# Kernel tuning notes

Hardware: AMD Instinct MI355X
Metric: run time of the kernel (lower is better)

## Reference

```python
import jax, jax.numpy as jnp
import numpy as np

BS, SEQ_Q = 16, 2048
ATTN_DIM, K_DIM, HEAD, RANK = 1024, 1024, 16, 16
A_H = ATTN_DIM // HEAD        # 64
K_R = K_DIM // RANK           # 64
HR = HEAD * RANK              # 256
EXP = 2
EPS = 1e-5


def setup_inputs() -> dict:
    key = jax.random.key(0)
    ks = jax.random.split(key, 12)
    n = lambda k, shape, scale=1.0: jax.random.normal(k, shape, dtype=jnp.float32) * scale
    lin = ATTN_DIM ** -0.5
    xav = (2.0 / (K_R + RANK)) ** 0.5  # xavier_normal for factor
    return {
        "Q": n(ks[0], (BS, SEQ_Q, ATTN_DIM)),
        "K": n(ks[1], (BS, K_DIM, ATTN_DIM)),
        "V": n(ks[2], (BS, K_DIM, ATTN_DIM)),
        "WQ": n(ks[3], (ATTN_DIM, ATTN_DIM), lin), "bQ": jnp.zeros((ATTN_DIM,), jnp.float32),
        "WK": n(ks[4], (ATTN_DIM, ATTN_DIM), lin), "bK": jnp.zeros((ATTN_DIM,), jnp.float32),
        "WV": n(ks[5], (ATTN_DIM, ATTN_DIM), lin), "bV": jnp.zeros((ATTN_DIM,), jnp.float32),
        "factor": n(ks[6], (1, A_H, K_R, RANK), xav),
        "W1": n(ks[7], (EXP * ATTN_DIM, ATTN_DIM), lin), "b1": jnp.zeros((EXP * ATTN_DIM,), jnp.float32),
        "W2": n(ks[8], (ATTN_DIM, EXP * ATTN_DIM), (EXP * ATTN_DIM) ** -0.5), "b2": jnp.zeros((ATTN_DIM,), jnp.float32),
        "gamma": jnp.ones((ATTN_DIM,), jnp.float32),
        "beta": jnp.zeros((ATTN_DIM,), jnp.float32),
    }


def reference(Q, K, V, WQ, bQ, WK, bK, WV, bV, factor, W1, b1, W2, b2, gamma, beta):
    bs = Q.shape[0]
    fac = factor[0]  # [a_h, k_r, rank]
    # Q path: [bs, a_h, head*rank, seq_q/rank]
    q = (Q @ WQ.T + bQ).reshape(bs, A_H, HR, -1)
    # K/V path: low-rank projection via learned factor -> [bs, a_h, head*rank, rank]
    k = jnp.einsum('bahk,akr->bahr', (K @ WK.T + bK).reshape(bs, A_H, HR, K_R), fac)
    v = jnp.einsum('bahk,akr->bahr', (V @ WV.T + bV).reshape(bs, A_H, HR, K_R), fac)
    # scores: Q^T K / sqrt(head*rank) -> [bs, a_h, L, rank]
    scores = jnp.einsum('bahl,bahr->balr', q, k) / jnp.float32(HR) ** 0.5
    attn = jax.nn.softmax(scores, axis=-1)
    # attn @ V^T -> [bs, a_h, L, head*rank], then flatten back to [bs, seq_q, attn_dim]
    ctx = jnp.einsum('balr,bahr->balh', attn, v).reshape(bs, -1, ATTN_DIM)
    # FFN (dropout = identity in eval)
    h = jax.nn.relu(ctx @ W1.T + b1)
    y = h @ W2.T + b2
    # residual + LayerNorm
    x = y + Q
    mu = jnp.mean(x, axis=-1, keepdims=True)
    var = jnp.var(x, axis=-1, keepdims=True)
    return (x - mu) * jax.lax.rsqrt(var + EPS) * gamma + beta
```

## Files before the change

### kernel.cpp

```cpp
#include <hip/hip_runtime.h>
#include <cstdint>

typedef unsigned short u16;
typedef unsigned int   u32;
typedef u16    u16x4  __attribute__((ext_vector_type(4)));
typedef u16    u16x8  __attribute__((ext_vector_type(8)));
typedef __bf16 bf16x8 __attribute__((ext_vector_type(8)));
typedef float  f32x4  __attribute__((ext_vector_type(4)));

__device__ __forceinline__ u16 f2b(float x) {
  u32 u = __builtin_bit_cast(u32, x);
  u32 r = (u + 0x7fffu + ((u >> 16) & 1u)) >> 16;
  return (u16)r;
}
__device__ __forceinline__ float b2f(u16 u) {
  return __builtin_bit_cast(float, (u32)u << 16);
}

__device__ __forceinline__ void gl2lds16(const u16* g, u16* l) {
  __builtin_amdgcn_global_load_lds(
      (__attribute__((address_space(1))) void*)g,
      (__attribute__((address_space(3))) void*)l, 16, 0, 0);
}

__global__ __launch_bounds__(256) void cvt_f32_bf16(
    const float* __restrict__ in, u16* __restrict__ out, long n)
{
  long i = ((long)blockIdx.x * 256 + threadIdx.x) * 4;
  if (i >= n) return;
  f32x4 v = *(const f32x4*)&in[i];
  u16x4 o = { f2b(v[0]), f2b(v[1]), f2b(v[2]), f2b(v[3]) };
  *(u16x4*)&out[i] = o;
}

#define BM 128
#define BN 128
#define BKK 32

__global__ __launch_bounds__(256) void gemm_bt(
    const u16* __restrict__ A, const u16* __restrict__ B,
    const float* __restrict__ bias, u16* __restrict__ C,
    int M, int N, int K, int relu)
{
  __shared__ __attribute__((aligned(16))) u16 As[BM * BKK];
  __shared__ __attribute__((aligned(16))) u16 Bs[BN * BKK];

  const int tid  = threadIdx.x;
  const int lane = tid & 63;
  const int wave = tid >> 6;
  const int lr   = lane & 15;
  const int quad = lane >> 4;
  const int wm = (wave >> 1) * 64;
  const int wn = (wave & 1) * 64;

  const long m0 = (long)blockIdx.y * BM;
  const long n0 = (long)blockIdx.x * BN;

  const int c1  = tid + 256;
  const int ar0 = tid >> 2, ac0 = (tid & 3) * 8;
  const int ar1 = c1 >> 2,  ac1 = (c1 & 3) * 8;

  const u16* Ab = A + m0 * K;
  const u16* Bb = B + n0 * K;

  f32x4 acc[4][4] = {};

  for (int k0 = 0; k0 < K; k0 += BKK) {
    __syncthreads();
    gl2lds16(Ab + (long)ar0 * K + (k0 + ac0), &As[tid * 8]);
    gl2lds16(Ab + (long)ar1 * K + (k0 + ac1), &As[c1 * 8]);
    gl2lds16(Bb + (long)ar0 * K + (k0 + ac0), &Bs[tid * 8]);
    gl2lds16(Bb + (long)ar1 * K + (k0 + ac1), &Bs[c1 * 8]);
    __syncthreads();

    bf16x8 af[4], bff[4];
#pragma unroll
    for (int i = 0; i < 4; ++i)
      af[i] = *(const bf16x8*)&As[(wm + i * 16 + lr) * BKK + quad * 8];
#pragma unroll
    for (int i = 0; i < 4; ++i)
      bff[i] = *(const bf16x8*)&Bs[(wn + i * 16 + lr) * BKK + quad * 8];
#pragma unroll
    for (int i = 0; i < 4; ++i)
#pragma unroll
      for (int j = 0; j < 4; ++j)
        acc[i][j] = __builtin_amdgcn_mfma_f32_16x16x32_bf16(af[i], bff[j], acc[i][j], 0, 0, 0);
  }

#pragma unroll
  for (int j = 0; j < 4; ++j) {
    const int col = wn + j * 16 + lr;
    const float bv = bias[n0 + col];
#pragma unroll
    for (int i = 0; i < 4; ++i) {
#pragma unroll
      for (int r = 0; r < 4; ++r) {
        const int row = wm + i * 16 + quad * 4 + r;
        float v = acc[i][j][r] + bv;
        if (relu) v = fmaxf(v, 0.0f);
        C[(m0 + row) * (long)N + (n0 + col)] = f2b(v);
      }
    }
  }
}

__global__ __launch_bounds__(256) void attn_kernel(
    const u16* __restrict__ Qp, const u16* __restrict__ Kp,
    const u16* __restrict__ Vp, const float* __restrict__ factor,
    u16* __restrict__ Ctx)
{
  __shared__ __attribute__((aligned(16))) float fac_s[64 * 16];
  __shared__ __attribute__((aligned(16))) float k_s[256][20];
  __shared__ __attribute__((aligned(16))) float v_s[256][20];
  __shared__ __attribute__((aligned(16))) float s_s[128][20];

  const int t = threadIdx.x;
  const int b = blockIdx.x >> 6;
  const int a = blockIdx.x & 63;

  for (int i = t; i < 1024; i += 256) fac_s[i] = factor[a * 1024 + i];
  __syncthreads();

  {
    const long kb = (((long)(b * 1024 + a * 16)) << 10) + (long)t * 64;
    float kacc[16] = {}, vacc[16] = {};
    for (int kk8 = 0; kk8 < 64; kk8 += 8) {
      u16x8 kv8 = *(const u16x8*)&Kp[kb + kk8];
      u16x8 vv8 = *(const u16x8*)&Vp[kb + kk8];
#pragma unroll
      for (int j = 0; j < 8; ++j) {
        const float kv = b2f(kv8[j]), vv = b2f(vv8[j]);
        const float* fr = &fac_s[(kk8 + j) * 16];
#pragma unroll
        for (int r = 0; r < 16; ++r) { kacc[r] += kv * fr[r]; vacc[r] += vv * fr[r]; }
      }
    }
#pragma unroll
    for (int r = 0; r < 16; ++r) { k_s[t][r] = kacc[r] * 0.0625f; v_s[t][r] = vacc[r]; }
  }
  __syncthreads();

  {
    const int l = t & 127, half = t >> 7;
    const long qb = (((long)(b * 2048 + a * 32)) << 10) + l;
    f32x4 acc0 = {}, acc1 = {};
    for (int h = 0; h < 256; ++h) {
      const float qv = b2f(Qp[qb + (long)h * 128]);
      f32x4 k0 = *(const f32x4*)&k_s[h][half * 8];
      f32x4 k1 = *(const f32x4*)&k_s[h][half * 8 + 4];
      acc0 += k0 * qv;
      acc1 += k1 * qv;
    }
    *(f32x4*)&s_s[l][half * 8]     = acc0;
    *(f32x4*)&s_s[l][half * 8 + 4] = acc1;
  }
  __syncthreads();

  if (t < 128) {
    float vals[16];
    float m = -1e30f;
#pragma unroll
    for (int r = 0; r < 16; ++r) { vals[r] = s_s[t][r]; m = fmaxf(m, vals[r]); }
    float sum = 0.0f;
#pragma unroll
    for (int r = 0; r < 16; ++r) { vals[r] = __expf(vals[r] - m); sum += vals[r]; }
    const float inv = 1.0f / sum;
#pragma unroll
    for (int r = 0; r < 16; ++r) s_s[t][r] = vals[r] * inv;
  }
  __syncthreads();

  {
    f32x4 v0 = *(const f32x4*)&v_s[t][0];
    f32x4 v1 = *(const f32x4*)&v_s[t][4];
    f32x4 v2 = *(const f32x4*)&v_s[t][8];
    f32x4 v3 = *(const f32x4*)&v_s[t][12];
    const long cb = (((long)(b * 2048 + a * 32)) << 10) + t;
    for (int l = 0; l < 128; ++l) {
      f32x4 a0 = *(const f32x4*)&s_s[l][0];
      f32x4 a1 = *(const f32x4*)&s_s[l][4];
      f32x4 a2 = *(const f32x4*)&s_s[l][8];
      f32x4 a3 = *(const f32x4*)&s_s[l][12];
      f32x4 p = a0 * v0 + a1 * v1 + a2 * v2 + a3 * v3;
      Ctx[cb + (long)l * 256] = f2b(p[0] + p[1] + p[2] + p[3]);
    }
  }
}

__global__ __launch_bounds__(256) void ln_kernel(
    const u16* __restrict__ Y, const float* __restrict__ Qin,
    const float* __restrict__ gamma, const float* __restrict__ beta,
    float* __restrict__ out)
{
  const long row = blockIdx.x;
  const int t = threadIdx.x;
  const long base = (row << 10) + (long)t * 4;

  u16x4 y4 = *(const u16x4*)&Y[base];
  f32x4 q4 = *(const f32x4*)&Qin[base];
  f32x4 x;
#pragma unroll
  for (int c = 0; c < 4; ++c) x[c] = b2f(y4[c]) + q4[c];

  float s  = x[0] + x[1] + x[2] + x[3];
  float sq = x[0]*x[0] + x[1]*x[1] + x[2]*x[2] + x[3]*x[3];
#pragma unroll
  for (int o = 1; o < 64; o <<= 1) {
    s  += __shfl_xor(s, o);
    sq += __shfl_xor(sq, o);
  }
  __shared__ float red[8];
  if ((t & 63) == 0) { red[(t >> 6) * 2] = s; red[(t >> 6) * 2 + 1] = sq; }
  __syncthreads();
  s  = red[0] + red[2] + red[4] + red[6];
  sq = red[1] + red[3] + red[5] + red[7];

  const float mean = s * (1.0f / 1024.0f);
  const float var  = sq * (1.0f / 1024.0f) - mean * mean;
  const float rstd = rsqrtf(var + 1e-5f);

  f32x4 g4 = *(const f32x4*)&gamma[t * 4];
  f32x4 be4 = *(const f32x4*)&beta[t * 4];
  f32x4 o4;
#pragma unroll
  for (int c = 0; c < 4; ++c) o4[c] = (x[c] - mean) * rstd * g4[c] + be4[c];
  *(f32x4*)&out[base] = o4;
}

extern "C" void kernel_launch(void* const* d_in, const int* in_sizes, int n_in,
                              void* d_out, int out_size, void* d_ws, size_t ws_size,
                              hipStream_t stream)
{
  (void)in_sizes; (void)n_in; (void)out_size; (void)ws_size;
  const float* Q      = (const float*)d_in[0];
  const float* K      = (const float*)d_in[1];
  const float* V      = (const float*)d_in[2];
  const float* WQ     = (const float*)d_in[3];
  const float* bQ     = (const float*)d_in[4];
  const float* WK     = (const float*)d_in[5];
  const float* bK     = (const float*)d_in[6];
  const float* WV     = (const float*)d_in[7];
  const float* bV     = (const float*)d_in[8];
  const float* factor = (const float*)d_in[9];
  const float* W1     = (const float*)d_in[10];
  const float* b1     = (const float*)d_in[11];
  const float* W2     = (const float*)d_in[12];
  const float* b2     = (const float*)d_in[13];
  const float* gamma  = (const float*)d_in[14];
  const float* beta   = (const float*)d_in[15];
  float* out = (float*)d_out;

  const long NQ = 33554432L;
  const long NK = 16777216L;
  const long ND = 1048576L;
  const long NW = 2097152L;

  char* w = (char*)d_ws;
  u16* Qb  = (u16*)(w);
  u16* Kb  = (u16*)(w + 67108864L);
  u16* Vb  = (u16*)(w + 100663296L);
  u16* WQb = (u16*)(w + 134217728L);
  u16* WKb = (u16*)(w + 136314880L);
  u16* WVb = (u16*)(w + 138412032L);
  u16* W1b = (u16*)(w + 140509184L);
  u16* W2b = (u16*)(w + 144703488L);
  u16* Qp  = (u16*)(w + 148897792L);
  u16* Kp  = (u16*)(w + 216006656L);
  u16* Vp  = (u16*)(w + 249561088L);
  u16* Ctx = (u16*)(w + 283115520L);
  u16* Hb  = (u16*)(w);
  u16* Yb  = (u16*)(w + 216006656L);

  cvt_f32_bf16<<<(int)(NQ / 1024), 256, 0, stream>>>(Q,  Qb,  NQ);
  cvt_f32_bf16<<<(int)(NK / 1024), 256, 0, stream>>>(K,  Kb,  NK);
  cvt_f32_bf16<<<(int)(NK / 1024), 256, 0, stream>>>(V,  Vb,  NK);
  cvt_f32_bf16<<<(int)(ND / 1024), 256, 0, stream>>>(WQ, WQb, ND);
  cvt_f32_bf16<<<(int)(ND / 1024), 256, 0, stream>>>(WK, WKb, ND);
  cvt_f32_bf16<<<(int)(ND / 1024), 256, 0, stream>>>(WV, WVb, ND);
  cvt_f32_bf16<<<(int)(NW / 1024), 256, 0, stream>>>(W1, W1b, NW);
  cvt_f32_bf16<<<(int)(NW / 1024), 256, 0, stream>>>(W2, W2b, NW);

  gemm_bt<<<dim3(8, 256),  256, 0, stream>>>(Qb, WQb, bQ, Qp, 32768, 1024, 1024, 0);
  gemm_bt<<<dim3(8, 128),  256, 0, stream>>>(Kb, WKb, bK, Kp, 16384, 1024, 1024, 0);
  gemm_bt<<<dim3(8, 128),  256, 0, stream>>>(Vb, WVb, bV, Vp, 16384, 1024, 1024, 0);

  attn_kernel<<<1024, 256, 0, stream>>>(Qp, Kp, Vp, factor, Ctx);

  gemm_bt<<<dim3(16, 256), 256, 0, stream>>>(Ctx, W1b, b1, Hb, 32768, 2048, 1024, 1);
  gemm_bt<<<dim3(8, 256),  256, 0, stream>>>(Hb, W2b, b2, Yb, 32768, 1024, 2048, 0);

  ln_kernel<<<32768, 256, 0, stream>>>(Yb, Q, gamma, beta, out);
}
```

Before: 1.120 ms.

## Merge conversion launches, deepen GEMM K-tile, swizzle LDS, group block order

The eight fp32-to-bf16 conversion launches become one kernel that uses segment offsets to pick the source and destination. The GEMM K-tile doubles from 32 to 64, halving the number of barrier pairs per output tile. LDS rows get an XOR swizzle to avoid bank conflicts on the 128-byte row stride. Blocks are remapped so groups of eight M-tiles run together for better L2 reuse. LDS use doubles to 32KB per block, which could lower occupancy.

```diff
diff --git a/kernel.cpp b/kernel.cpp
--- a/kernel.cpp
+++ b/kernel.cpp
@@ -23,27 +23,38 @@
       (__attribute__((address_space(3))) void*)l, 16, 0, 0);
 }
 
-__global__ __launch_bounds__(256) void cvt_f32_bf16(
-    const float* __restrict__ in, u16* __restrict__ out, long n)
-{
-  long i = ((long)blockIdx.x * 256 + threadIdx.x) * 4;
-  if (i >= n) return;
-  f32x4 v = *(const f32x4*)&in[i];
+struct CvtArgs {
+  const float* src[8];
+  u16*         dst[8];
+  long         end[8];
+};
+
+__global__ __launch_bounds__(256) void cvt_all(CvtArgs a)
+{
+  long g = (long)blockIdx.x * 1024;
+  int seg = 0;
+#pragma unroll
+  for (int s = 0; s < 8; ++s) seg += (g >= a.end[s]) ? 1 : 0;
+  long base = (seg == 0) ? 0 : a.end[seg - 1];
+  long off = g - base + (long)threadIdx.x * 4;
+  const float* src = a.src[seg];
+  u16* dst = a.dst[seg];
+  f32x4 v = *(const f32x4*)&src[off];
   u16x4 o = { f2b(v[0]), f2b(v[1]), f2b(v[2]), f2b(v[3]) };
-  *(u16x4*)&out[i] = o;
+  *(u16x4*)&dst[off] = o;
 }
 
 #define BM 128
 #define BN 128
-#define BKK 32
+#define BK 64
 
 __global__ __launch_bounds__(256) void gemm_bt(
     const u16* __restrict__ A, const u16* __restrict__ B,
     const float* __restrict__ bias, u16* __restrict__ C,
     int M, int N, int K, int relu)
 {
-  __shared__ __attribute__((aligned(16))) u16 As[BM * BKK];
-  __shared__ __attribute__((aligned(16))) u16 Bs[BN * BKK];
+  __shared__ __attribute__((aligned(16))) u16 As[BM * BK];
+  __shared__ __attribute__((aligned(16))) u16 Bs[BN * BK];
 
   const int tid  = threadIdx.x;
   const int lane = tid & 63;
@@ -53,38 +64,58 @@
   const int wm = (wave >> 1) * 64;
   const int wn = (wave & 1) * 64;
 
-  const long m0 = (long)blockIdx.y * BM;
-  const long n0 = (long)blockIdx.x * BN;
-
-  const int c1  = tid + 256;
-  const int ar0 = tid >> 2, ac0 = (tid & 3) * 8;
-  const int ar1 = c1 >> 2,  ac1 = (c1 & 3) * 8;
+  const int Nb = gridDim.x;
+  const int flat = blockIdx.y * Nb + blockIdx.x;
+  const int sg  = flat / (8 * Nb);
+  const int rem = flat - sg * 8 * Nb;
+  const int bx  = rem >> 3;
+  const int by  = sg * 8 + (rem & 7);
+
+  const long m0 = (long)by * BM;
+  const long n0 = (long)bx * BN;
+
+  long goff[4];
+#pragma unroll
+  for (int c = 0; c < 4; ++c) {
+    const int p = tid + 256 * c;
+    const int row = p >> 3;
+    const int logcol = (p & 7) ^ (row & 7);
+    goff[c] = (long)row * K + logcol * 8;
+  }
 
   const u16* Ab = A + m0 * K;
   const u16* Bb = B + n0 * K;
 
+  const int ph0 = quad ^ (lane & 7);
+  const int ph1 = (quad + 4) ^ (lane & 7);
+
   f32x4 acc[4][4] = {};
 
-  for (int k0 = 0; k0 < K; k0 += BKK) {
+  for (int k0 = 0; k0 < K; k0 += BK) {
     __syncthreads();
-    gl2lds16(Ab + (long)ar0 * K + (k0 + ac0), &As[tid * 8]);
-    gl2lds16(Ab + (long)ar1 * K + (k0 + ac1), &As[c1 * 8]);
-    gl2lds16(Bb + (long)ar0 * K + (k0 + ac0), &Bs[tid * 8]);
-    gl2lds16(Bb + (long)ar1 * K + (k0 + ac1), &Bs[c1 * 8]);
+#pragma unroll
+    for (int c = 0; c < 4; ++c) {
+      gl2lds16(Ab + goff[c] + k0, &As[(tid + 256 * c) * 8]);
+      gl2lds16(Bb + goff[c] + k0, &Bs[(tid + 256 * c) * 8]);
+    }
     __syncthreads();
 
-    bf16x8 af[4], bff[4];
-#pragma unroll
-    for (int i = 0; i < 4; ++i)
-      af[i] = *(const bf16x8*)&As[(wm + i * 16 + lr) * BKK + quad * 8];
-#pragma unroll
-    for (int i = 0; i < 4; ++i)
-      bff[i] = *(const bf16x8*)&Bs[(wn + i * 16 + lr) * BKK + quad * 8];
-#pragma unroll
-    for (int i = 0; i < 4; ++i)
-#pragma unroll
-      for (int j = 0; j < 4; ++j)
-        acc[i][j] = __builtin_amdgcn_mfma_f32_16x16x32_bf16(af[i], bff[j], acc[i][j], 0, 0, 0);
+#pragma unroll
+    for (int kh = 0; kh < 2; ++kh) {
+      const int ph = kh ? ph1 : ph0;
+      bf16x8 af[4], bff[4];
+#pragma unroll
+      for (int i = 0; i < 4; ++i)
+        af[i] = *(const bf16x8*)&As[(wm + i * 16 + lr) * BK + ph * 8];
+#pragma unroll
+      for (int i = 0; i < 4; ++i)
+        bff[i] = *(const bf16x8*)&Bs[(wn + i * 16 + lr) * BK + ph * 8];
+#pragma unroll
+      for (int i = 0; i < 4; ++i)
+#pragma unroll
+        for (int j = 0; j < 4; ++j)
+          acc[i][j] = __builtin_amdgcn_mfma_f32_16x16x32_bf16(af[i], bff[j], acc[i][j], 0, 0, 0);
+    }
   }
 
 #pragma unroll
@@ -271,14 +302,19 @@
   u16* Hb  = (u16*)(w);
   u16* Yb  = (u16*)(w + 216006656L);
 
-  cvt_f32_bf16<<<(int)(NQ / 1024), 256, 0, stream>>>(Q,  Qb,  NQ);
-  cvt_f32_bf16<<<(int)(NK / 1024), 256, 0, stream>>>(K,  Kb,  NK);
-  cvt_f32_bf16<<<(int)(NK / 1024), 256, 0, stream>>>(V,  Vb,  NK);
-  cvt_f32_bf16<<<(int)(ND / 1024), 256, 0, stream>>>(WQ, WQb, ND);
-  cvt_f32_bf16<<<(int)(ND / 1024), 256, 0, stream>>>(WK, WKb, ND);
-  cvt_f32_bf16<<<(int)(ND / 1024), 256, 0, stream>>>(WV, WVb, ND);
-  cvt_f32_bf16<<<(int)(NW / 1024), 256, 0, stream>>>(W1, W1b, NW);
-  cvt_f32_bf16<<<(int)(NW / 1024), 256, 0, stream>>>(W2, W2b, NW);
+  CvtArgs ca;
+  ca.src[0] = Q;  ca.dst[0] = Qb;
+  ca.src[1] = K;  ca.dst[1] = Kb;
+  ca.src[2] = V;  ca.dst[2] = Vb;
+  ca.src[3] = WQ; ca.dst[3] = WQb;
+  ca.src[4] = WK; ca.dst[4] = WKb;
+  ca.src[5] = WV; ca.dst[5] = WVb;
+  ca.src[6] = W1; ca.dst[6] = W1b;
+  ca.src[7] = W2; ca.dst[7] = W2b;
+  long sizes[8] = { NQ, NK, NK, ND, ND, ND, NW, NW };
+  long cum = 0;
+  for (int i = 0; i < 8; ++i) { cum += sizes[i]; ca.end[i] = cum; }
+  cvt_all<<<(int)(cum / 1024), 256, 0, stream>>>(ca);
 
   gemm_bt<<<dim3(8, 256),  256, 0, stream>>>(Qb, WQb, bQ, Qp, 32768, 1024, 1024, 0);
   gemm_bt<<<dim3(8, 128),  256, 0, stream>>>(Kb, WKb, bK, Kp, 16384, 1024, 1024, 0);
```

After: 1.057 ms. -5.6%, faster.
